# Optimization experiments

Measured on AMD Instinct MI355X. Metric: run time of the kernel, lower is better.

Reference implementation:

```python
import jax, jax.numpy as jnp
import numpy as np

# per-head local window sizes (== init local_region_shape); all divide H=W=64 -> no boundary masks
REGIONS = (4, 4, 8, 8, 16, 16, 32, 32)


def setup_inputs() -> dict:
    key = jax.random.key(0)
    ks = jax.random.split(key, 4)
    B, H, W, C = 4, 64, 64, 512
    N = H * W
    std = 0.02  # trunc_normal_(std=0.02) in the torch init
    return {
        "x": jax.random.normal(ks[0], (B, N, C), jnp.float32),
        "Wq": jax.random.normal(ks[1], (C, C), jnp.float32) * std,
        "Wkv": jax.random.normal(ks[2], (C, 2 * C), jnp.float32) * std,
        "Wproj": jax.random.normal(ks[3], (C, C), jnp.float32) * std,
        "bproj": jnp.zeros((C,), jnp.float32),
        "H": 64,
        "W": 64,
    }


def _to_windows(xh, H, W, r):
    # (B, N, d) -> (B*Hr*Wr, r*r, d), windows in row-major order (matches F.unfold k=stride=r)
    B, N, d = xh.shape
    Hr, Wr = H // r, W // r
    x = xh.reshape(B, Hr, r, Wr, r, d).transpose(0, 1, 3, 2, 4, 5)
    return x.reshape(B * Hr * Wr, r * r, d)


def _from_windows(xw, B, H, W, r):
    # inverse of _to_windows (matches F.fold k=stride=r)
    d = xw.shape[-1]
    Hr, Wr = H // r, W // r
    x = xw.reshape(B, Hr, Wr, r, r, d).transpose(0, 1, 3, 2, 4, 5)
    return x.reshape(B, H * W, d)


def reference(x, Wq, Wkv, Wproj, bproj, H, W):
    B, N, C = x.shape
    nh = len(REGIONS)
    hd = C // nh
    scale = hd ** -0.5
    q = (x @ Wq).reshape(B, N, nh, hd).transpose(0, 2, 1, 3)            # (B, nh, N, hd)
    kv = (x @ Wkv).reshape(B, N, 2, nh, hd).transpose(2, 0, 3, 1, 4)    # (2, B, nh, N, hd)
    k, v = kv[0], kv[1]
    outs = []
    for i, r in enumerate(REGIONS):
        qh, kh, vh = q[:, i], k[:, i], v[:, i]                          # (B, N, hd)
        if r == 1:
            attn = jax.nn.softmax(jnp.einsum("bqd,bkd->bqk", qh, kh) * scale, axis=-1)
            outs.append(jnp.einsum("bqk,bkd->bqd", attn, vh))
        else:
            qw = _to_windows(qh, H, W, r)                               # (B*nw, r*r, hd)
            kw = _to_windows(kh, H, W, r)
            vw = _to_windows(vh, H, W, r)
            attn = jax.nn.softmax(jnp.einsum("wqd,wkd->wqk", qw, kw) * scale, axis=-1)
            ow = jnp.einsum("wqk,wkd->wqd", attn, vw)
            outs.append(_from_windows(ow, B, H, W, r))
    o = jnp.stack(outs, axis=2).reshape(B, N, C)                        # heads interleaved per token
    return o @ Wproj + bproj
```

## Files before the change

### kernel.cpp

```cpp
#include <hip/hip_runtime.h>

typedef unsigned short ushort_t;
typedef __attribute__((ext_vector_type(4))) float f32x4;
typedef __attribute__((ext_vector_type(8))) short s16x8;
typedef __attribute__((ext_vector_type(4))) unsigned int u32x4;

#define LOG2E 1.44269504088896340736f

__device__ inline unsigned short bf16_rne(float f) {
    unsigned u = __builtin_bit_cast(unsigned, f);
    unsigned r = u + 0x7FFFu + ((u >> 16) & 1u);
    return (unsigned short)(r >> 16);
}

__device__ inline f32x4 mfma16(s16x8 a, s16x8 b, f32x4 c) {
    return __builtin_amdgcn_mfma_f32_16x16x32_bf16(a, b, c, 0, 0, 0);
}


__global__ __launch_bounds__(256) void cvt_x_kernel(const float* __restrict__ x,
                                                    unsigned short* __restrict__ xb, int n8) {
    int i = blockIdx.x * 256 + threadIdx.x;
    if (i >= n8) return;
    const float4* xp = (const float4*)x + (size_t)i * 2;
    float4 a = xp[0], b = xp[1];
    unsigned short r[8] = {bf16_rne(a.x), bf16_rne(a.y), bf16_rne(a.z), bf16_rne(a.w),
                           bf16_rne(b.x), bf16_rne(b.y), bf16_rne(b.z), bf16_rne(b.w)};
    *(u32x4*)(xb + (size_t)i * 8) = *(u32x4*)r;
}

__global__ __launch_bounds__(256) void cvt_t_kernel(const float* __restrict__ src,
                                                    unsigned short* __restrict__ dst, int Rr, int Cc) {
    int i = blockIdx.x * 256 + threadIdx.x;
    if (i >= Rr * Cc) return;
    int r = i / Cc, c = i % Cc;
    dst[(size_t)c * Rr + r] = bf16_rne(src[i]);
}


template <int OUTF>
__global__ __launch_bounds__(256) void gemm128(const unsigned short* __restrict__ A,
                                               const unsigned short* __restrict__ BT,
                                               void* __restrict__ Cv,
                                               const float* __restrict__ bias,
                                               int M, int N, int K) {
    __shared__ unsigned short Alds[128 * 64];
    __shared__ unsigned short Blds[128 * 64];
    const int t = threadIdx.x, lane = t & 63, wv = t >> 6;
    const int wm = wv >> 1, wn = wv & 1;
    const int tm = blockIdx.y, tn = blockIdx.x;

    f32x4 acc[4][4];
#pragma unroll
    for (int mf = 0; mf < 4; mf++)
#pragma unroll
        for (int nf = 0; nf < 4; nf++) acc[mf][nf] = f32x4{0.f, 0.f, 0.f, 0.f};

    const int nkt = K >> 6;
    for (int kt = 0; kt < nkt; kt++) {
        __syncthreads();
#pragma unroll
        for (int i = 0; i < 4; i++) {
            int ul = i * 256 + t;
            int row = ul >> 3, u = ul & 7;
            u32x4 av = *(const u32x4*)(A + (size_t)(tm * 128 + row) * K + kt * 64 + u * 8);
            *(u32x4*)((char*)Alds + row * 128 + ((u ^ (row & 7)) << 4)) = av;
            u32x4 bv = *(const u32x4*)(BT + (size_t)(tn * 128 + row) * K + kt * 64 + u * 8);
            *(u32x4*)((char*)Blds + row * 128 + ((u ^ (row & 7)) << 4)) = bv;
        }
        __syncthreads();
#pragma unroll
        for (int ks = 0; ks < 2; ks++) {
            s16x8 af[4], bf[4];
#pragma unroll
            for (int mf = 0; mf < 4; mf++) {
                int row = wm * 64 + mf * 16 + (lane & 15);
                af[mf] = *(const s16x8*)((char*)Alds + row * 128 +
                                         ((((ks << 2) | (lane >> 4)) ^ (row & 7)) << 4));
            }
#pragma unroll
            for (int nf = 0; nf < 4; nf++) {
                int row = wn * 64 + nf * 16 + (lane & 15);
                bf[nf] = *(const s16x8*)((char*)Blds + row * 128 +
                                         ((((ks << 2) | (lane >> 4)) ^ (row & 7)) << 4));
            }
#pragma unroll
            for (int mf = 0; mf < 4; mf++)
#pragma unroll
                for (int nf = 0; nf < 4; nf++) acc[mf][nf] = mfma16(af[mf], bf[nf], acc[mf][nf]);
        }
    }

#pragma unroll
    for (int mf = 0; mf < 4; mf++) {
#pragma unroll
        for (int r = 0; r < 4; r++) {
            int row = tm * 128 + wm * 64 + mf * 16 + (lane >> 4) * 4 + r;
#pragma unroll
            for (int nf = 0; nf < 4; nf++) {
                int col = tn * 128 + wn * 64 + nf * 16 + (lane & 15);
                float v = acc[mf][nf][r];
                if constexpr (OUTF) {
                    ((float*)Cv)[(size_t)row * N + col] = v + bias[col];
                } else {
                    ((unsigned short*)Cv)[(size_t)row * N + col] = bf16_rne(v);
                }
            }
        }
    }
}


template <int R>
__global__ __launch_bounds__(256) void attn_win(const unsigned short* __restrict__ qkv,
                                                unsigned short* __restrict__ ob) {
    constexpr int L = R * R;
    constexpr int NCH = L / 64;
    constexpr int WPD = 64 / R;
    constexpr int NWIN = WPD * WPD;
    constexpr int HEAD0 = (R == 8) ? 2 : ((R == 16) ? 4 : 6);

    __shared__ unsigned short Klds[64 * 64];
    __shared__ unsigned short VTlds[64 * 64];
    __shared__ unsigned short Plds[4][16 * 64];

    const int t = threadIdx.x;
    const int lane = t & 63;
    const int wv = t >> 6;

    const int bpw = L / 64;
    int g = blockIdx.x;
    int wid = g / bpw;
    int qc = g % bpw;
    int w = wid % NWIN;
    int hb = wid / NWIN;
    int b = hb & 3;
    int head = HEAD0 + (hb >> 2);
    int wy = w / WPD, wx = w % WPD;

    const unsigned short* qbase = qkv + (size_t)b * 4096 * 1536;

    int qrow_w = qc * 64 + wv * 16 + (lane & 15);
    int qn = (wy * R + qrow_w / R) * 64 + wx * R + qrow_w % R;
    s16x8 qf[2];
    {
        const unsigned short* qp = qbase + (size_t)qn * 1536 + head * 64 + (lane >> 4) * 8;
        qf[0] = *(const s16x8*)(qp);
        qf[1] = *(const s16x8*)(qp + 32);
    }

    f32x4 o[4];
    float mrun[4], lrun[4];
#pragma unroll
    for (int i = 0; i < 4; i++) {
        o[i] = f32x4{0.f, 0.f, 0.f, 0.f};
        mrun[i] = -1e30f;
        lrun[i] = 0.f;
    }

    for (int c = 0; c < NCH; c++) {
        __syncthreads();
#pragma unroll
        for (int i = 0; i < 2; i++) {
            int ul = i * 256 + t;
            int tok = ul >> 3, u = ul & 7;
            int tw = c * 64 + tok;
            int n = (wy * R + tw / R) * 64 + wx * R + tw % R;
            u32x4 d = *(const u32x4*)(qbase + (size_t)n * 1536 + 512 + head * 64 + u * 8);
            *(u32x4*)((char*)Klds + tok * 128 + ((u ^ (tok & 7)) << 4)) = d;
        }
        {
            int tok = t & 63, dgrp = t >> 6;
            int tw = c * 64 + tok;
            int n = (wy * R + tw / R) * 64 + wx * R + tw % R;
            const unsigned short* vp = qbase + (size_t)n * 1536 + 1024 + head * 64;
#pragma unroll
            for (int i = 0; i < 2; i++) {
                int dim0 = dgrp * 8 + i * 32;
                u32x4 d = *(const u32x4*)(vp + dim0);
                const unsigned short* dsv = (const unsigned short*)&d;
#pragma unroll
                for (int j = 0; j < 8; j++) {
                    int dim = dim0 + j;
                    *(unsigned short*)((char*)VTlds + dim * 128 +
                                       ((((tok >> 3) ^ (dim & 7))) << 4) + (tok & 7) * 2) = dsv[j];
                }
            }
        }
        __syncthreads();

        f32x4 s[4];
#pragma unroll
        for (int cf = 0; cf < 4; cf++) s[cf] = f32x4{0.f, 0.f, 0.f, 0.f};
#pragma unroll
        for (int ks = 0; ks < 2; ks++) {
#pragma unroll
            for (int cf = 0; cf < 4; cf++) {
                int tok = cf * 16 + (lane & 15);
                s16x8 kb = *(const s16x8*)((char*)Klds + tok * 128 +
                                           ((((ks << 2) | (lane >> 4)) ^ (tok & 7)) << 4));
                s[cf] = mfma16(qf[ks], kb, s[cf]);
            }
        }
#pragma unroll
        for (int cf = 0; cf < 4; cf++) s[cf] *= 0.125f;

        float pm[4];
#pragma unroll
        for (int r = 0; r < 4; r++)
            pm[r] = fmaxf(fmaxf(s[0][r], s[1][r]), fmaxf(s[2][r], s[3][r]));
#pragma unroll
        for (int m = 1; m < 16; m <<= 1)
#pragma unroll
            for (int r = 0; r < 4; r++) pm[r] = fmaxf(pm[r], __shfl_xor(pm[r], m, 64));

        float mnew[4], corr[4];
#pragma unroll
        for (int r = 0; r < 4; r++) {
            mnew[r] = fmaxf(mrun[r], pm[r]);
            corr[r] = exp2f((mrun[r] - mnew[r]) * LOG2E);
            mrun[r] = mnew[r];
        }
        float rs[4] = {0.f, 0.f, 0.f, 0.f};
        unsigned short pu[4][4];
#pragma unroll
        for (int cf = 0; cf < 4; cf++)
#pragma unroll
            for (int r = 0; r < 4; r++) {
                float p = exp2f((s[cf][r] - mnew[r]) * LOG2E);
                rs[r] += p;
                pu[cf][r] = bf16_rne(p);
            }
#pragma unroll
        for (int m = 1; m < 16; m <<= 1)
#pragma unroll
            for (int r = 0; r < 4; r++) rs[r] += __shfl_xor(rs[r], m, 64);
#pragma unroll
        for (int r = 0; r < 4; r++) lrun[r] = lrun[r] * corr[r] + rs[r];
#pragma unroll
        for (int nf = 0; nf < 4; nf++)
#pragma unroll
            for (int r = 0; r < 4; r++) o[nf][r] *= corr[r];

        unsigned short* pw = Plds[wv];
#pragma unroll
        for (int cf = 0; cf < 4; cf++) {
            int col = cf * 16 + (lane & 15);
#pragma unroll
            for (int r = 0; r < 4; r++) {
                int row = (lane >> 4) * 4 + r;
                *(unsigned short*)((char*)pw + row * 128 + (((col >> 3) ^ (row & 7)) << 4) +
                                   (col & 7) * 2) = pu[cf][r];
            }
        }
        asm volatile("s_waitcnt lgkmcnt(0)" ::: "memory");

#pragma unroll
        for (int ks = 0; ks < 2; ks++) {
            int prow = lane & 15;
            s16x8 pa = *(const s16x8*)((char*)pw + prow * 128 +
                                       ((((ks << 2) | (lane >> 4)) ^ (prow & 7)) << 4));
#pragma unroll
            for (int nf = 0; nf < 4; nf++) {
                int dim = nf * 16 + (lane & 15);
                s16x8 vb = *(const s16x8*)((char*)VTlds + dim * 128 +
                                           ((((ks << 2) | (lane >> 4)) ^ (dim & 7)) << 4));
                o[nf] = mfma16(pa, vb, o[nf]);
            }
        }
    }

#pragma unroll
    for (int r = 0; r < 4; r++) {
        int qr = qc * 64 + wv * 16 + (lane >> 4) * 4 + r;
        int n = (wy * R + qr / R) * 64 + wx * R + qr % R;
        float inv = 1.0f / lrun[r];
        unsigned short* op = ob + ((size_t)b * 4096 + n) * 512 + head * 64 + (lane & 15);
#pragma unroll
        for (int nf = 0; nf < 4; nf++) op[nf * 16] = bf16_rne(o[nf][r] * inv);
    }
}


__global__ __launch_bounds__(256) void attn_win4(const unsigned short* __restrict__ qkv,
                                                 unsigned short* __restrict__ ob) {
    __shared__ unsigned short VTlds[4][64 * 32];
    __shared__ unsigned short Plds[4][16 * 32];
    const int t = threadIdx.x, lane = t & 63, wv = t >> 6;
    int gwin = blockIdx.x * 4 + wv;
    int w = gwin & 255;
    int hb = gwin >> 8;
    int b = hb & 3;
    int head = hb >> 2;
    int wy = w >> 4, wx = w & 15;
    const unsigned short* qbase = qkv + (size_t)b * 4096 * 1536;

    int qtok = lane & 15;
    int qn = (wy * 4 + (qtok >> 2)) * 64 + wx * 4 + (qtok & 3);
    const unsigned short* qp = qbase + (size_t)qn * 1536 + head * 64 + (lane >> 4) * 8;
    s16x8 qf0 = *(const s16x8*)(qp);
    s16x8 qf1 = *(const s16x8*)(qp + 32);

    int kn = qn;
    const unsigned short* kp = qbase + (size_t)kn * 1536 + 512 + head * 64 + (lane >> 4) * 8;
    s16x8 kb0 = *(const s16x8*)(kp);
    s16x8 kb1 = *(const s16x8*)(kp + 32);

    f32x4 s = f32x4{0.f, 0.f, 0.f, 0.f};
    s = mfma16(qf0, kb0, s);
    s = mfma16(qf1, kb1, s);
    s *= 0.125f;

    unsigned short* vt = VTlds[wv];
    {
        int tok = lane & 15, dgrp = lane >> 4;
        int vn = (wy * 4 + (tok >> 2)) * 64 + wx * 4 + (tok & 3);
        const unsigned short* vp = qbase + (size_t)vn * 1536 + 1024 + head * 64;
#pragma unroll
        for (int i = 0; i < 2; i++) {
            int dim0 = dgrp * 8 + i * 32;
            u32x4 d = *(const u32x4*)(vp + dim0);
            const unsigned short* dsv = (const unsigned short*)&d;
#pragma unroll
            for (int j = 0; j < 8; j++) {
                int dim = dim0 + j;
                vt[dim * 32 + tok] = dsv[j];
                vt[dim * 32 + 16 + tok] = 0;
            }
        }
    }

    float pm[4];
#pragma unroll
    for (int r = 0; r < 4; r++) pm[r] = s[r];
#pragma unroll
    for (int m = 1; m < 16; m <<= 1)
#pragma unroll
        for (int r = 0; r < 4; r++) pm[r] = fmaxf(pm[r], __shfl_xor(pm[r], m, 64));

    float l4[4];
    unsigned short pu[4];
#pragma unroll
    for (int r = 0; r < 4; r++) {
        float p = exp2f((s[r] - pm[r]) * LOG2E);
        pu[r] = bf16_rne(p);
        l4[r] = p;
    }
#pragma unroll
    for (int m = 1; m < 16; m <<= 1)
#pragma unroll
        for (int r = 0; r < 4; r++) l4[r] += __shfl_xor(l4[r], m, 64);

    unsigned short* pl = Plds[wv];
#pragma unroll
    for (int r = 0; r < 4; r++) {
        int row = (lane >> 4) * 4 + r;
        pl[row * 32 + (lane & 15)] = pu[r];
        pl[row * 32 + 16 + (lane & 15)] = 0;
    }
    asm volatile("s_waitcnt lgkmcnt(0)" ::: "memory");

    s16x8 pa = *(const s16x8*)(pl + (lane & 15) * 32 + (lane >> 4) * 8);
    f32x4 o[4];
#pragma unroll
    for (int nf = 0; nf < 4; nf++) {
        s16x8 vb = *(const s16x8*)(vt + (nf * 16 + (lane & 15)) * 32 + (lane >> 4) * 8);
        o[nf] = mfma16(pa, vb, f32x4{0.f, 0.f, 0.f, 0.f});
    }

#pragma unroll
    for (int r = 0; r < 4; r++) {
        int qr = (lane >> 4) * 4 + r;
        int n = (wy * 4 + (qr >> 2)) * 64 + wx * 4 + (qr & 3);
        float inv = 1.0f / l4[r];
        unsigned short* op = ob + ((size_t)b * 4096 + n) * 512 + head * 64 + (lane & 15);
#pragma unroll
        for (int nf = 0; nf < 4; nf++) op[nf * 16] = bf16_rne(o[nf][r] * inv);
    }
}


extern "C" void kernel_launch(void* const* d_in, const int* in_sizes, int n_in,
                              void* d_out, int out_size, void* d_ws, size_t ws_size,
                              hipStream_t stream) {
    (void)in_sizes; (void)n_in; (void)out_size; (void)ws_size;
    const float* x = (const float*)d_in[0];
    const float* Wq = (const float*)d_in[1];
    const float* Wkv = (const float*)d_in[2];
    const float* Wproj = (const float*)d_in[3];
    const float* bproj = (const float*)d_in[4];

    char* ws = (char*)d_ws;
    unsigned short* qkv = (unsigned short*)ws;
    unsigned short* xb = (unsigned short*)(ws + (size_t)16384 * 1536 * 2);
    unsigned short* WcatT = (unsigned short*)(ws + (size_t)16384 * 1536 * 2 + (size_t)16384 * 512 * 2);
    unsigned short* WprojT = WcatT + (size_t)1536 * 512;
    unsigned short* ob = xb;

    cvt_x_kernel<<<4096, 256, 0, stream>>>(x, xb, 16384 * 512 / 8);
    cvt_t_kernel<<<1024, 256, 0, stream>>>(Wq, WcatT, 512, 512);
    cvt_t_kernel<<<2048, 256, 0, stream>>>(Wkv, WcatT + (size_t)512 * 512, 512, 1024);
    cvt_t_kernel<<<1024, 256, 0, stream>>>(Wproj, WprojT, 512, 512);

    gemm128<0><<<dim3(12, 128), 256, 0, stream>>>(xb, WcatT, (void*)qkv, nullptr, 16384, 1536, 512);

    attn_win4<<<512, 256, 0, stream>>>(qkv, ob);
    attn_win<8><<<512, 256, 0, stream>>>(qkv, ob);
    attn_win<16><<<512, 256, 0, stream>>>(qkv, ob);
    attn_win<32><<<512, 256, 0, stream>>>(qkv, ob);

    gemm128<1><<<dim3(4, 128), 256, 0, stream>>>(ob, WprojT, d_out, bproj, 16384, 512, 512);
}
```

Baseline: 226.9 us.

## Fuse attention launches, write V transposed from GEMM, use direct global-to-LDS loads

The QKV GEMM epilogue now writes V in a transposed layout to a separate buffer, and Q/K are stored with a 1024 stride. The three weight-conversion kernels are merged into one, and the four attention kernels become a single launch that dispatches on block index. The windowed attention loads K and V fragments straight from global memory instead of staging them through LDS with block barriers. The GEMM uses global_load_lds to fill shared memory directly. This removes launches, LDS transposes and syncs, at the cost of uncoalesced transposed stores in the GEMM and more scattered global reads in attention.

```diff
diff --git a/kernel.cpp b/kernel.cpp
--- a/kernel.cpp
+++ b/kernel.cpp
@@ -1,11 +1,15 @@
 #include <hip/hip_runtime.h>
 
-typedef unsigned short ushort_t;
 typedef __attribute__((ext_vector_type(4))) float f32x4;
 typedef __attribute__((ext_vector_type(8))) short s16x8;
 typedef __attribute__((ext_vector_type(4))) unsigned int u32x4;
+typedef __attribute__((ext_vector_type(2))) unsigned int u32x2;
 
 #define LOG2E 1.44269504088896340736f
+
+#define GLOAD_LDS16(g, l)                                                     \
+    __builtin_amdgcn_global_load_lds((const __attribute__((address_space(1))) void*)(g), \
+                                     (__attribute__((address_space(3))) void*)(l), 16, 0, 0)
 
 __device__ inline unsigned short bf16_rne(float f) {
     unsigned u = __builtin_bit_cast(unsigned, f);
@@ -29,25 +33,36 @@
     *(u32x4*)(xb + (size_t)i * 8) = *(u32x4*)r;
 }
 
-__global__ __launch_bounds__(256) void cvt_t_kernel(const float* __restrict__ src,
-                                                    unsigned short* __restrict__ dst, int Rr, int Cc) {
+__global__ __launch_bounds__(256) void cvt_w_kernel(const float* __restrict__ Wq,
+                                                    const float* __restrict__ Wkv,
+                                                    const float* __restrict__ Wproj,
+                                                    unsigned short* __restrict__ WcatT,
+                                                    unsigned short* __restrict__ WprojT) {
     int i = blockIdx.x * 256 + threadIdx.x;
-    if (i >= Rr * Cc) return;
-    int r = i / Cc, c = i % Cc;
-    dst[(size_t)c * Rr + r] = bf16_rne(src[i]);
-}
-
-
-template <int OUTF>
+    if (i < 786432) {
+        int n = i >> 9, k = i & 511;
+        float v = (n < 512) ? Wq[k * 512 + n] : Wkv[k * 1024 + (n - 512)];
+        WcatT[i] = bf16_rne(v);
+    } else {
+        int j = i - 786432;
+        int n = j >> 9, k = j & 511;
+        WprojT[j] = bf16_rne(Wproj[k * 512 + n]);
+    }
+}
+
+
+template <int MODE>
 __global__ __launch_bounds__(256) void gemm128(const unsigned short* __restrict__ A,
                                                const unsigned short* __restrict__ BT,
                                                void* __restrict__ Cv,
                                                const float* __restrict__ bias,
-                                               int M, int N, int K) {
+                                               unsigned short* __restrict__ vT,
+                                               int M, int K, int ldc) {
     __shared__ unsigned short Alds[128 * 64];
     __shared__ unsigned short Blds[128 * 64];
-    const int t = threadIdx.x, lane = t & 63, wv = t >> 6;
-    const int wm = wv >> 1, wn = wv & 1;
+    const int t = threadIdx.x, lane = t & 63;
+    const int wv4 = t >> 6;
+    const int wm = wv4 >> 1, wn = wv4 & 1;
     const int tm = blockIdx.y, tn = blockIdx.x;
 
     f32x4 acc[4][4];
@@ -61,12 +76,13 @@
         __syncthreads();
 #pragma unroll
         for (int i = 0; i < 4; i++) {
-            int ul = i * 256 + t;
-            int row = ul >> 3, u = ul & 7;
-            u32x4 av = *(const u32x4*)(A + (size_t)(tm * 128 + row) * K + kt * 64 + u * 8);
-            *(u32x4*)((char*)Alds + row * 128 + ((u ^ (row & 7)) << 4)) = av;
-            u32x4 bv = *(const u32x4*)(BT + (size_t)(tn * 128 + row) * K + kt * 64 + u * 8);
-            *(u32x4*)((char*)Blds + row * 128 + ((u ^ (row & 7)) << 4)) = bv;
+            int l = i * 256 + t;
+            int row = l >> 3, u = l & 7;
+            int us = u ^ (row & 7);
+            GLOAD_LDS16(A + (size_t)(tm * 128 + row) * K + kt * 64 + us * 8,
+                        (char*)Alds + l * 16);
+            GLOAD_LDS16(BT + (size_t)(tn * 128 + row) * K + kt * 64 + us * 8,
+                        (char*)Blds + l * 16);
         }
         __syncthreads();
 #pragma unroll
@@ -93,17 +109,26 @@
 
 #pragma unroll
     for (int mf = 0; mf < 4; mf++) {
-#pragma unroll
-        for (int r = 0; r < 4; r++) {
-            int row = tm * 128 + wm * 64 + mf * 16 + (lane >> 4) * 4 + r;
-#pragma unroll
-            for (int nf = 0; nf < 4; nf++) {
-                int col = tn * 128 + wn * 64 + nf * 16 + (lane & 15);
-                float v = acc[mf][nf][r];
-                if constexpr (OUTF) {
-                    ((float*)Cv)[(size_t)row * N + col] = v + bias[col];
+        int row0 = tm * 128 + wm * 64 + mf * 16 + (lane >> 4) * 4;
+#pragma unroll
+        for (int nf = 0; nf < 4; nf++) {
+            int col = tn * 128 + wn * 64 + nf * 16 + (lane & 15);
+            if constexpr (MODE == 1) {
+                float bb = bias[col];
+#pragma unroll
+                for (int r = 0; r < 4; r++)
+                    ((float*)Cv)[(size_t)(row0 + r) * ldc + col] = acc[mf][nf][r] + bb;
+            } else {
+                if (tn < 8) {
+#pragma unroll
+                    for (int r = 0; r < 4; r++)
+                        ((unsigned short*)Cv)[(size_t)(row0 + r) * ldc + col] =
+                            bf16_rne(acc[mf][nf][r]);
                 } else {
-                    ((unsigned short*)Cv)[(size_t)row * N + col] = bf16_rne(v);
+                    unsigned short tmp[4];
+#pragma unroll
+                    for (int r = 0; r < 4; r++) tmp[r] = bf16_rne(acc[mf][nf][r]);
+                    *(u32x2*)(vT + (size_t)(col - 1024) * 16384 + row0) = *(u32x2*)tmp;
                 }
             }
         }
@@ -112,42 +137,34 @@
 
 
 template <int R>
-__global__ __launch_bounds__(256) void attn_win(const unsigned short* __restrict__ qkv,
-                                                unsigned short* __restrict__ ob) {
-    constexpr int L = R * R;
-    constexpr int NCH = L / 64;
+__device__ __forceinline__ void attn_body(int g, const unsigned short* __restrict__ qkv,
+                                          const unsigned short* __restrict__ vT,
+                                          unsigned short* __restrict__ ob,
+                                          char* smem, int lane, int wv) {
+    constexpr int lR = (R == 8) ? 3 : ((R == 16) ? 4 : 5);
+    constexpr int NCH = (R * R) / 64;
     constexpr int WPD = 64 / R;
     constexpr int NWIN = WPD * WPD;
     constexpr int HEAD0 = (R == 8) ? 2 : ((R == 16) ? 4 : 6);
-
-    __shared__ unsigned short Klds[64 * 64];
-    __shared__ unsigned short VTlds[64 * 64];
-    __shared__ unsigned short Plds[4][16 * 64];
-
-    const int t = threadIdx.x;
-    const int lane = t & 63;
-    const int wv = t >> 6;
-
-    const int bpw = L / 64;
-    int g = blockIdx.x;
-    int wid = g / bpw;
-    int qc = g % bpw;
-    int w = wid % NWIN;
-    int hb = wid / NWIN;
-    int b = hb & 3;
-    int head = HEAD0 + (hb >> 2);
+    constexpr int BPW = (R * R) / 64;
+
+    int wid = g / BPW, qc = g % BPW;
+    int w = wid % NWIN, hb = wid / NWIN;
+    int b = hb & 3, head = HEAD0 + (hb >> 2);
     int wy = w / WPD, wx = w % WPD;
 
-    const unsigned short* qbase = qkv + (size_t)b * 4096 * 1536;
-
-    int qrow_w = qc * 64 + wv * 16 + (lane & 15);
-    int qn = (wy * R + qrow_w / R) * 64 + wx * R + qrow_w % R;
-    s16x8 qf[2];
-    {
-        const unsigned short* qp = qbase + (size_t)qn * 1536 + head * 64 + (lane >> 4) * 8;
-        qf[0] = *(const s16x8*)(qp);
-        qf[1] = *(const s16x8*)(qp + 32);
-    }
+    const int lc = lane & 15, lg = lane >> 4;
+    const unsigned short* qbase = qkv + (size_t)b * 4096 * 1024;
+    const unsigned short* vbase = vT + (size_t)head * 64 * 16384 + b * 4096;
+    const int wbase = wy * R * 64 + wx * R;
+
+    int qrow = qc * 64 + wv * 16 + lc;
+    int qn = wbase + (qrow >> lR) * 64 + (qrow & (R - 1));
+    const unsigned short* qp = qbase + (size_t)qn * 1024 + head * 64 + lg * 8;
+    s16x8 qf0 = *(const s16x8*)qp;
+    s16x8 qf1 = *(const s16x8*)(qp + 32);
+
+    unsigned short* pw = (unsigned short*)smem + wv * (16 * 64);
 
     f32x4 o[4];
     float mrun[4], lrun[4];
@@ -159,48 +176,18 @@
     }
 
     for (int c = 0; c < NCH; c++) {
-        __syncthreads();
-#pragma unroll
-        for (int i = 0; i < 2; i++) {
-            int ul = i * 256 + t;
-            int tok = ul >> 3, u = ul & 7;
-            int tw = c * 64 + tok;
-            int n = (wy * R + tw / R) * 64 + wx * R + tw % R;
-            u32x4 d = *(const u32x4*)(qbase + (size_t)n * 1536 + 512 + head * 64 + u * 8);
-            *(u32x4*)((char*)Klds + tok * 128 + ((u ^ (tok & 7)) << 4)) = d;
-        }
-        {
-            int tok = t & 63, dgrp = t >> 6;
-            int tw = c * 64 + tok;
-            int n = (wy * R + tw / R) * 64 + wx * R + tw % R;
-            const unsigned short* vp = qbase + (size_t)n * 1536 + 1024 + head * 64;
-#pragma unroll
-            for (int i = 0; i < 2; i++) {
-                int dim0 = dgrp * 8 + i * 32;
-                u32x4 d = *(const u32x4*)(vp + dim0);
-                const unsigned short* dsv = (const unsigned short*)&d;
-#pragma unroll
-                for (int j = 0; j < 8; j++) {
-                    int dim = dim0 + j;
-                    *(unsigned short*)((char*)VTlds + dim * 128 +
-                                       ((((tok >> 3) ^ (dim & 7))) << 4) + (tok & 7) * 2) = dsv[j];
-                }
-            }
-        }
-        __syncthreads();
-
         f32x4 s[4];
 #pragma unroll
         for (int cf = 0; cf < 4; cf++) s[cf] = f32x4{0.f, 0.f, 0.f, 0.f};
 #pragma unroll
-        for (int ks = 0; ks < 2; ks++) {
-#pragma unroll
-            for (int cf = 0; cf < 4; cf++) {
-                int tok = cf * 16 + (lane & 15);
-                s16x8 kb = *(const s16x8*)((char*)Klds + tok * 128 +
-                                           ((((ks << 2) | (lane >> 4)) ^ (tok & 7)) << 4));
-                s[cf] = mfma16(qf[ks], kb, s[cf]);
-            }
+        for (int cf = 0; cf < 4; cf++) {
+            int tok = c * 64 + cf * 16 + lc;
+            int n = wbase + (tok >> lR) * 64 + (tok & (R - 1));
+            const unsigned short* kp = qbase + (size_t)n * 1024 + 512 + head * 64 + lg * 8;
+            s16x8 kb0 = *(const s16x8*)kp;
+            s16x8 kb1 = *(const s16x8*)(kp + 32);
+            s[cf] = mfma16(qf0, kb0, s[cf]);
+            s[cf] = mfma16(qf1, kb1, s[cf]);
         }
 #pragma unroll
         for (int cf = 0; cf < 4; cf++) s[cf] *= 0.125f;
@@ -242,29 +229,28 @@
 #pragma unroll
             for (int r = 0; r < 4; r++) o[nf][r] *= corr[r];
 
-        unsigned short* pw = Plds[wv];
 #pragma unroll
         for (int cf = 0; cf < 4; cf++) {
-            int col = cf * 16 + (lane & 15);
+            int col = cf * 16 + lc;
 #pragma unroll
             for (int r = 0; r < 4; r++) {
-                int row = (lane >> 4) * 4 + r;
+                int row = lg * 4 + r;
                 *(unsigned short*)((char*)pw + row * 128 + (((col >> 3) ^ (row & 7)) << 4) +
                                    (col & 7) * 2) = pu[cf][r];
             }
         }
         asm volatile("s_waitcnt lgkmcnt(0)" ::: "memory");
+        __builtin_amdgcn_sched_barrier(0);
 
 #pragma unroll
         for (int ks = 0; ks < 2; ks++) {
-            int prow = lane & 15;
-            s16x8 pa = *(const s16x8*)((char*)pw + prow * 128 +
-                                       ((((ks << 2) | (lane >> 4)) ^ (prow & 7)) << 4));
+            s16x8 pa = *(const s16x8*)((char*)pw + lc * 128 +
+                                       ((((ks << 2) | lg) ^ (lc & 7)) << 4));
+            int tok0 = c * 64 + ks * 32 + lg * 8;
+            int n0 = wbase + (tok0 >> lR) * 64 + (tok0 & (R - 1));
 #pragma unroll
             for (int nf = 0; nf < 4; nf++) {
-                int dim = nf * 16 + (lane & 15);
-                s16x8 vb = *(const s16x8*)((char*)VTlds + dim * 128 +
-                                           ((((ks << 2) | (lane >> 4)) ^ (dim & 7)) << 4));
+                s16x8 vb = *(const s16x8*)(vbase + (size_t)(nf * 16 + lc) * 16384 + n0);
                 o[nf] = mfma16(pa, vb, o[nf]);
             }
         }
@@ -272,38 +258,35 @@
 
 #pragma unroll
     for (int r = 0; r < 4; r++) {
-        int qr = qc * 64 + wv * 16 + (lane >> 4) * 4 + r;
-        int n = (wy * R + qr / R) * 64 + wx * R + qr % R;
+        int qr = qc * 64 + wv * 16 + lg * 4 + r;
+        int n = wbase + (qr >> lR) * 64 + (qr & (R - 1));
         float inv = 1.0f / lrun[r];
-        unsigned short* op = ob + ((size_t)b * 4096 + n) * 512 + head * 64 + (lane & 15);
+        unsigned short* op = ob + ((size_t)b * 4096 + n) * 512 + head * 64 + lc;
 #pragma unroll
         for (int nf = 0; nf < 4; nf++) op[nf * 16] = bf16_rne(o[nf][r] * inv);
     }
 }
 
-
-__global__ __launch_bounds__(256) void attn_win4(const unsigned short* __restrict__ qkv,
-                                                 unsigned short* __restrict__ ob) {
-    __shared__ unsigned short VTlds[4][64 * 32];
-    __shared__ unsigned short Plds[4][16 * 32];
-    const int t = threadIdx.x, lane = t & 63, wv = t >> 6;
-    int gwin = blockIdx.x * 4 + wv;
-    int w = gwin & 255;
-    int hb = gwin >> 8;
-    int b = hb & 3;
-    int head = hb >> 2;
+__device__ __forceinline__ void attn4_body(int g, const unsigned short* __restrict__ qkv,
+                                           const unsigned short* __restrict__ vT,
+                                           unsigned short* __restrict__ ob,
+                                           char* smem, int lane, int wv) {
+    unsigned short* vt = (unsigned short*)smem + wv * (64 * 32);
+    unsigned short* pl = (unsigned short*)(smem + 16384) + wv * (16 * 32);
+    const int lc = lane & 15, lg = lane >> 4;
+
+    int gwin = g * 4 + wv;
+    int w = gwin & 255, hb = gwin >> 8;
+    int b = hb & 3, head = hb >> 2;
     int wy = w >> 4, wx = w & 15;
-    const unsigned short* qbase = qkv + (size_t)b * 4096 * 1536;
-
-    int qtok = lane & 15;
-    int qn = (wy * 4 + (qtok >> 2)) * 64 + wx * 4 + (qtok & 3);
-    const unsigned short* qp = qbase + (size_t)qn * 1536 + head * 64 + (lane >> 4) * 8;
-    s16x8 qf0 = *(const s16x8*)(qp);
+    const unsigned short* qbase = qkv + (size_t)b * 4096 * 1024;
+
+    int qn = (wy * 4 + (lc >> 2)) * 64 + wx * 4 + (lc & 3);
+    const unsigned short* qp = qbase + (size_t)qn * 1024 + head * 64 + lg * 8;
+    s16x8 qf0 = *(const s16x8*)qp;
     s16x8 qf1 = *(const s16x8*)(qp + 32);
-
-    int kn = qn;
-    const unsigned short* kp = qbase + (size_t)kn * 1536 + 512 + head * 64 + (lane >> 4) * 8;
-    s16x8 kb0 = *(const s16x8*)(kp);
+    const unsigned short* kp = qbase + (size_t)qn * 1024 + 512 + head * 64 + lg * 8;
+    s16x8 kb0 = *(const s16x8*)kp;
     s16x8 kb1 = *(const s16x8*)(kp + 32);
 
     f32x4 s = f32x4{0.f, 0.f, 0.f, 0.f};
@@ -311,23 +294,19 @@
     s = mfma16(qf1, kb1, s);
     s *= 0.125f;
 
-    unsigned short* vt = VTlds[wv];
     {
-        int tok = lane & 15, dgrp = lane >> 4;
-        int vn = (wy * 4 + (tok >> 2)) * 64 + wx * 4 + (tok & 3);
-        const unsigned short* vp = qbase + (size_t)vn * 1536 + 1024 + head * 64;
-#pragma unroll
-        for (int i = 0; i < 2; i++) {
-            int dim0 = dgrp * 8 + i * 32;
-            u32x4 d = *(const u32x4*)(vp + dim0);
-            const unsigned short* dsv = (const unsigned short*)&d;
-#pragma unroll
-            for (int j = 0; j < 8; j++) {
-                int dim = dim0 + j;
-                vt[dim * 32 + tok] = dsv[j];
-                vt[dim * 32 + 16 + tok] = 0;
-            }
-        }
+        int d = lane;
+        const unsigned short* vp = vT + (size_t)(head * 64 + d) * 16384 + b * 4096;
+        char* vrow = (char*)vt + d * 64;
+#pragma unroll
+        for (int tr = 0; tr < 4; tr++) {
+            int n0 = (wy * 4 + tr) * 64 + wx * 4;
+            u32x2 dv = *(const u32x2*)(vp + n0);
+            *(u32x2*)(vrow + (((tr >> 1) ^ (d & 3)) << 4) + (tr & 1) * 8) = dv;
+        }
+        u32x4 z = u32x4{0, 0, 0, 0};
+        *(u32x4*)(vrow + ((2 ^ (d & 3)) << 4)) = z;
+        *(u32x4*)(vrow + ((3 ^ (d & 3)) << 4)) = z;
     }
 
     float pm[4];
@@ -351,32 +330,45 @@
 #pragma unroll
         for (int r = 0; r < 4; r++) l4[r] += __shfl_xor(l4[r], m, 64);
 
-    unsigned short* pl = Plds[wv];
 #pragma unroll
     for (int r = 0; r < 4; r++) {
-        int row = (lane >> 4) * 4 + r;
-        pl[row * 32 + (lane & 15)] = pu[r];
-        pl[row * 32 + 16 + (lane & 15)] = 0;
+        int row = lg * 4 + r;
+        pl[row * 32 + lc] = pu[r];
+        pl[row * 32 + 16 + lc] = 0;
     }
     asm volatile("s_waitcnt lgkmcnt(0)" ::: "memory");
-
-    s16x8 pa = *(const s16x8*)(pl + (lane & 15) * 32 + (lane >> 4) * 8);
+    __builtin_amdgcn_sched_barrier(0);
+
+    s16x8 pa = *(const s16x8*)(pl + lc * 32 + lg * 8);
     f32x4 o[4];
 #pragma unroll
     for (int nf = 0; nf < 4; nf++) {
-        s16x8 vb = *(const s16x8*)(vt + (nf * 16 + (lane & 15)) * 32 + (lane >> 4) * 8);
+        int dim = nf * 16 + lc;
+        s16x8 vb = *(const s16x8*)((char*)vt + dim * 64 + ((lg ^ (dim & 3)) << 4));
         o[nf] = mfma16(pa, vb, f32x4{0.f, 0.f, 0.f, 0.f});
     }
 
 #pragma unroll
     for (int r = 0; r < 4; r++) {
-        int qr = (lane >> 4) * 4 + r;
+        int qr = lg * 4 + r;
         int n = (wy * 4 + (qr >> 2)) * 64 + wx * 4 + (qr & 3);
         float inv = 1.0f / l4[r];
-        unsigned short* op = ob + ((size_t)b * 4096 + n) * 512 + head * 64 + (lane & 15);
+        unsigned short* op = ob + ((size_t)b * 4096 + n) * 512 + head * 64 + lc;
 #pragma unroll
         for (int nf = 0; nf < 4; nf++) op[nf * 16] = bf16_rne(o[nf][r] * inv);
     }
+}
+
+__global__ __launch_bounds__(256) void attn_all(const unsigned short* __restrict__ qkv,
+                                                const unsigned short* __restrict__ vT,
+                                                unsigned short* __restrict__ ob) {
+    __shared__ __align__(16) char smem[20480];
+    int t = threadIdx.x, lane = t & 63, wv = t >> 6;
+    int g = blockIdx.x;
+    if (g < 512) attn_body<32>(g, qkv, vT, ob, smem, lane, wv);
+    else if (g < 1024) attn_body<16>(g - 512, qkv, vT, ob, smem, lane, wv);
+    else if (g < 1536) attn_body<8>(g - 1024, qkv, vT, ob, smem, lane, wv);
+    else attn4_body(g - 1536, qkv, vT, ob, smem, lane, wv);
 }
 
 
@@ -392,22 +384,20 @@
 
     char* ws = (char*)d_ws;
     unsigned short* qkv = (unsigned short*)ws;
-    unsigned short* xb = (unsigned short*)(ws + (size_t)16384 * 1536 * 2);
-    unsigned short* WcatT = (unsigned short*)(ws + (size_t)16384 * 1536 * 2 + (size_t)16384 * 512 * 2);
+    unsigned short* vT = (unsigned short*)(ws + (((size_t)32) << 20));
+    unsigned short* xb = (unsigned short*)(ws + (((size_t)48) << 20));
+    unsigned short* WcatT = (unsigned short*)(ws + (((size_t)64) << 20));
     unsigned short* WprojT = WcatT + (size_t)1536 * 512;
     unsigned short* ob = xb;
 
     cvt_x_kernel<<<4096, 256, 0, stream>>>(x, xb, 16384 * 512 / 8);
-    cvt_t_kernel<<<1024, 256, 0, stream>>>(Wq, WcatT, 512, 512);
-    cvt_t_kernel<<<2048, 256, 0, stream>>>(Wkv, WcatT + (size_t)512 * 512, 512, 1024);
-    cvt_t_kernel<<<1024, 256, 0, stream>>>(Wproj, WprojT, 512, 512);
-
-    gemm128<0><<<dim3(12, 128), 256, 0, stream>>>(xb, WcatT, (void*)qkv, nullptr, 16384, 1536, 512);
-
-    attn_win4<<<512, 256, 0, stream>>>(qkv, ob);
-    attn_win<8><<<512, 256, 0, stream>>>(qkv, ob);
-    attn_win<16><<<512, 256, 0, stream>>>(qkv, ob);
-    attn_win<32><<<512, 256, 0, stream>>>(qkv, ob);
-
-    gemm128<1><<<dim3(4, 128), 256, 0, stream>>>(ob, WprojT, d_out, bproj, 16384, 512, 512);
-}
+    cvt_w_kernel<<<4096, 256, 0, stream>>>(Wq, Wkv, Wproj, WcatT, WprojT);
+
+    gemm128<0><<<dim3(12, 128), 256, 0, stream>>>(xb, WcatT, (void*)qkv, nullptr, vT,
+                                                  16384, 512, 1024);
+
+    attn_all<<<2048, 256, 0, stream>>>(qkv, vT, ob);
+
+    gemm128<1><<<dim3(4, 128), 256, 0, stream>>>(ob, WprojT, d_out, bproj, nullptr,
+                                                 16384, 512, 512);
+}
```

After: 239.4 us. 1.06x slower.
